# Performance work log

Hardware: AMD Instinct MI355X
Metric: run time of the kernel (lower is better)

Reference implementation:

```python
import jax, jax.numpy as jnp
import numpy as np

B, T, H = 32, 1024, 1024


def setup_inputs() -> dict:
    key = jax.random.key(0)
    k1, k2, k3, k4, k5 = jax.random.split(key, 5)
    h_t = jax.random.normal(k1, (B, H), dtype=jnp.float32)
    enc_out = jax.random.normal(k2, (B, T, H), dtype=jnp.float32)
    src_mask = jnp.ones((B, T), dtype=bool)
    s = 1.0 / np.sqrt(H)
    Wa = jax.random.normal(k3, (H, H), dtype=jnp.float32) * s
    Ua = jax.random.normal(k4, (H, H), dtype=jnp.float32) * s
    va = jax.random.normal(k5, (H,), dtype=jnp.float32) * s
    return {"h_t": h_t, "enc_out": enc_out, "src_mask": src_mask,
            "Wa": Wa, "Ua": Ua, "va": va}


def reference(h_t, enc_out, src_mask, Wa, Ua, va):
    # h_proj: [B,H] ; enc_proj: [B,T,H]
    h_proj = h_t @ Wa.T
    enc_proj = jnp.einsum('bth,kh->btk', enc_out, Ua)
    # additive score: va . tanh(Wa h + Ua enc)  -> [B,T]
    e = jnp.einsum('bth,h->bt', jnp.tanh(h_proj[:, None, :] + enc_proj), va)
    e = jnp.where(src_mask, e, -jnp.inf)
    attn = jax.nn.softmax(e, axis=1)                     # [B,T]
    context = jnp.einsum('bt,bth->bh', attn, enc_out)    # [B,H]
    return context, attn
```

## Files before the change

### kernel.cpp

```cpp
#include <hip/hip_runtime.h>

#define BB 32
#define TT 1024
#define HH 1024
#define MM (BB * TT)

typedef __bf16 bf16x8 __attribute__((ext_vector_type(8)));
typedef float  f32x4  __attribute__((ext_vector_type(4)));

__device__ __forceinline__ void async_copy16(const void* g, void* l) {
  __builtin_amdgcn_global_load_lds(
      (const __attribute__((address_space(1))) void*)g,
      (__attribute__((address_space(3))) void*)l, 16, 0, 0);
}

__device__ __forceinline__ float fast_tanh(float x) {
  float e2 = __expf(2.f * x);
  return 1.f - 2.f * __builtin_amdgcn_rcpf(e2 + 1.f);
}

__global__ __launch_bounds__(256) void mini_prep_kernel(
    const float* __restrict__ Ua, const float* __restrict__ h_t,
    const float* __restrict__ Wa, __bf16* __restrict__ uab,
    float* __restrict__ hp, float* __restrict__ e) {
  const int blk = blockIdx.x;
  const int tid = threadIdx.x;

  if (blk < 128) {
    const int b = blk >> 2;
    const int k = (blk & 3) * 256 + tid;
    __shared__ float hs[HH];
    for (int i = tid; i < HH; i += 256) hs[i] = h_t[b * HH + i];
    __syncthreads();
    const float4* w  = (const float4*)(Wa + (size_t)k * HH);
    const float4* hv = (const float4*)hs;
    float acc = 0.f;
#pragma unroll 8
    for (int i = 0; i < HH / 4; ++i) {
      float4 a = w[i];
      float4 h = hv[i];
      acc += a.x * h.x + a.y * h.y + a.z * h.z + a.w * h.w;
    }
    hp[b * HH + k] = acc;
  } else if (blk < 256) {
    int F = (blk - 128) * 256 + tid;
#pragma unroll
    for (int it = 0; it < 4; ++it, F += 32768) {
      const int c   = F & 2047;
      const int t   = F >> 11;
      const int kt  = t & 15;
      const int rt  = t >> 4;
      const int u   = c >> 10;
      const int idx = (c >> 3) & 127;
      const int s   = c & 7;
      const int g   = s ^ (idx & 7);
      const int row = (idx & 63) + ((idx >> 6) & 1) * 128 + u * 64;
      const float* sp = Ua + (((size_t)rt * 256 + row) << 10) + (kt << 6) + (g << 3);
      f32x4 a  = *(const f32x4*)sp;
      f32x4 b2 = *(const f32x4*)(sp + 4);
      bf16x8 o;
      o[0] = (__bf16)a[0];  o[1] = (__bf16)a[1];
      o[2] = (__bf16)a[2];  o[3] = (__bf16)a[3];
      o[4] = (__bf16)b2[0]; o[5] = (__bf16)b2[1];
      o[6] = (__bf16)b2[2]; o[7] = (__bf16)b2[3];
      *(bf16x8*)(uab + (size_t)F * 8) = o;
    }
  } else {
    f32x4 z = {0.f, 0.f, 0.f, 0.f};
    f32x4* ep = (f32x4*)e;
#pragma unroll
    for (int i = 0; i < 32; ++i) ep[i * 256 + tid] = z;
  }
}

__global__ __launch_bounds__(128) void hproj_kernel(
    const float* __restrict__ h_t, const float* __restrict__ Wa,
    float* __restrict__ hp) {
  const int k = blockIdx.x * 128 + threadIdx.x;
  const int b = blockIdx.y;
  __shared__ float hs[HH];
  for (int i = threadIdx.x; i < HH; i += 128) hs[i] = h_t[b * HH + i];
  __syncthreads();
  const float4* w  = (const float4*)(Wa + (size_t)k * HH);
  const float4* hv = (const float4*)hs;
  float acc = 0.f;
#pragma unroll 8
  for (int i = 0; i < HH / 4; ++i) {
    float4 a = w[i];
    float4 h = hv[i];
    acc += a.x * h.x + a.y * h.y + a.z * h.z + a.w * h.w;
  }
  hp[b * HH + k] = acc;
}

__global__ __launch_bounds__(512, 1) void score_8ph_kernel(
    const float* __restrict__ enc, const __bf16* __restrict__ uab,
    const float* __restrict__ hp, const float* __restrict__ va,
    float* __restrict__ e) {
  __shared__ __bf16 As[2][16384];
  __shared__ __bf16 Bs[2][16384];

  const int wg = blockIdx.x;
  const int sw = (wg & 7) * 64 + (wg >> 3);
  const int nt = sw & 3;
  const int mt = sw >> 2;
  const int b  = mt >> 2;

  const int tid  = threadIdx.x;
  const int lane = tid & 63;
  const int wid  = tid >> 6;
  const int wr   = wid >> 2;
  const int wc   = wid & 3;
  const int rl   = lane & 15;
  const int kq   = lane >> 4;
  const int e7   = rl & 7;

  const float* Af = enc + ((size_t)(mt * 256) << 10);
  const __bf16* Bg = uab + ((size_t)(nt * 16) << 14);

  const int aidx = tid >> 3;
  const int ag8  = ((tid & 7) ^ (aidx & 7)) << 3;

  const int s0 = ((kq ^ e7) << 4);
  const int s1 = (((kq + 4) ^ e7) << 4);
  const int arow = (rl + wr * 64) * 128;
  const int brow = (rl + (wc >> 1) * 64) * 128 + (wc & 1) * 16384;

#define LDA(buf, mi, sl) (*(const bf16x8*)((const char*)(buf) + \
    (((mi) >> 2) * 16384 + ((mi) & 3) * 2048) + arow + (sl)))
#define LDB(buf, nj, sl) (*(const bf16x8*)((const char*)(buf) + \
    ((nj) * 2048) + brow + (sl)))

#define BSTAGE(kt2, lp, u) do { \
    const __bf16* _g = Bg + (((size_t)(kt2)) << 14) + (((u) << 10) + tid) * 8; \
    __bf16* _l = (lp) + (((u) << 10) + tid) * 8; \
    async_copy16(_g, _l); \
    async_copy16(_g + 4096, _l + 4096); \
  } while (0)

#define ALOAD(ra, rb, rc, rd, kt2, u) do { \
    const float* _p1 = Af + ((size_t)(aidx + (u) * 64) << 10) + ((kt2) << 6) + ag8; \
    const float* _p2 = _p1 + (128 << 10); \
    ra = *(const f32x4*)_p1; rb = *(const f32x4*)(_p1 + 4); \
    rc = *(const f32x4*)_p2; rd = *(const f32x4*)(_p2 + 4); \
  } while (0)

#define AWRITE(lp, u, ra, rb, rc, rd) do { \
    __bf16* _l = (lp) + ((u) << 13) + tid * 8; \
    bf16x8 o1, o2; \
    o1[0] = (__bf16)ra[0]; o1[1] = (__bf16)ra[1]; \
    o1[2] = (__bf16)ra[2]; o1[3] = (__bf16)ra[3]; \
    o1[4] = (__bf16)rb[0]; o1[5] = (__bf16)rb[1]; \
    o1[6] = (__bf16)rb[2]; o1[7] = (__bf16)rb[3]; \
    o2[0] = (__bf16)rc[0]; o2[1] = (__bf16)rc[1]; \
    o2[2] = (__bf16)rc[2]; o2[3] = (__bf16)rc[3]; \
    o2[4] = (__bf16)rd[0]; o2[5] = (__bf16)rd[1]; \
    o2[6] = (__bf16)rd[2]; o2[7] = (__bf16)rd[3]; \
    *(bf16x8*)_l = o1; \
    *(bf16x8*)(_l + 4096) = o2; \
  } while (0)

#define MFMA16(ml, kkb) do { \
    _Pragma("unroll") \
    for (int nj = 0; nj < 4; ++nj) { \
      acc[(ml) + 0][nj] = __builtin_amdgcn_mfma_f32_16x16x32_bf16(af0, bfr[(kkb) + nj], acc[(ml) + 0][nj], 0, 0, 0); \
      acc[(ml) + 1][nj] = __builtin_amdgcn_mfma_f32_16x16x32_bf16(af1, bfr[(kkb) + nj], acc[(ml) + 1][nj], 0, 0, 0); \
      acc[(ml) + 2][nj] = __builtin_amdgcn_mfma_f32_16x16x32_bf16(af2, bfr[(kkb) + nj], acc[(ml) + 2][nj], 0, 0, 0); \
      acc[(ml) + 3][nj] = __builtin_amdgcn_mfma_f32_16x16x32_bf16(af3, bfr[(kkb) + nj], acc[(ml) + 3][nj], 0, 0, 0); \
    } \
  } while (0)

  f32x4 acc[8][4] = {};
  bf16x8 bfr[8];
  f32x4 xa, xb, xc, xd;
  f32x4 ya, yb, yc, yd;

  ALOAD(xa, xb, xc, xd, 0, 0);
  BSTAGE(0, &Bs[0][0], 0);
  BSTAGE(0, &Bs[0][0], 1);
  ALOAD(ya, yb, yc, yd, 0, 1);
  BSTAGE(1, &Bs[1][0], 0);
  BSTAGE(1, &Bs[1][0], 1);
  asm volatile("s_waitcnt vmcnt(4)" ::: "memory");
  AWRITE(&As[0][0], 0, xa, xb, xc, xd);
  AWRITE(&As[0][0], 1, ya, yb, yc, yd);
  ALOAD(xa, xb, xc, xd, 1, 0);
  asm volatile("s_waitcnt lgkmcnt(0)" ::: "memory");
  __builtin_amdgcn_s_barrier();

  for (int t = 0; t < 15; ++t) {
    const int p = t & 1;
    const char* Ab = (const char*)&As[p][0];
    const char* Bb = (const char*)&Bs[p][0];
    __bf16* An = &As[p ^ 1][0];

    {
#pragma unroll
      for (int nj = 0; nj < 4; ++nj) { bfr[nj] = LDB(Bb, nj, s0); bfr[4 + nj] = LDB(Bb, nj, s1); }
      bf16x8 af0 = LDA(Ab, 0, s0), af1 = LDA(Ab, 1, s0), af2 = LDA(Ab, 2, s0), af3 = LDA(Ab, 3, s0);
      ALOAD(ya, yb, yc, yd, t + 1, 1);
      __builtin_amdgcn_s_barrier();
      asm volatile("s_waitcnt lgkmcnt(0)" ::: "memory");
      __builtin_amdgcn_s_setprio(1);
      MFMA16(0, 0);
      __builtin_amdgcn_s_setprio(0);
      __builtin_amdgcn_s_barrier();
    }
    {
      bf16x8 af0 = LDA(Ab, 0, s1), af1 = LDA(Ab, 1, s1), af2 = LDA(Ab, 2, s1), af3 = LDA(Ab, 3, s1);
      if (t < 14) BSTAGE(t + 2, &Bs[p][0], 0);
      __builtin_amdgcn_s_barrier();
      asm volatile("s_waitcnt lgkmcnt(0)" ::: "memory");
      __builtin_amdgcn_s_setprio(1);
      MFMA16(0, 4);
      __builtin_amdgcn_s_setprio(0);
      __builtin_amdgcn_s_barrier();
    }
    {
      bf16x8 af0 = LDA(Ab, 4, s0), af1 = LDA(Ab, 5, s0), af2 = LDA(Ab, 6, s0), af3 = LDA(Ab, 7, s0);
      if (t < 14) BSTAGE(t + 2, &Bs[p][0], 1);
      __builtin_amdgcn_s_barrier();
      asm volatile("s_waitcnt lgkmcnt(0)" ::: "memory");
      __builtin_amdgcn_s_setprio(1);
      MFMA16(4, 0);
      __builtin_amdgcn_s_setprio(0);
      __builtin_amdgcn_s_barrier();
    }
    {
      bf16x8 af0 = LDA(Ab, 4, s1), af1 = LDA(Ab, 5, s1), af2 = LDA(Ab, 6, s1), af3 = LDA(Ab, 7, s1);
      __builtin_amdgcn_s_barrier();
      asm volatile("s_waitcnt lgkmcnt(0)" ::: "memory");
      __builtin_amdgcn_s_setprio(1);
      MFMA16(4, 4);
      __builtin_amdgcn_s_setprio(0);
      if (t < 14) asm volatile("s_waitcnt vmcnt(4)" ::: "memory");
      else        asm volatile("s_waitcnt vmcnt(0)" ::: "memory");
      AWRITE(An, 0, xa, xb, xc, xd);
      AWRITE(An, 1, ya, yb, yc, yd);
      if (t < 14) ALOAD(xa, xb, xc, xd, t + 2, 0);
      asm volatile("s_waitcnt lgkmcnt(0)" ::: "memory");
      __builtin_amdgcn_s_barrier();
    }
  }

  {
    const char* Ab = (const char*)&As[1][0];
    const char* Bb = (const char*)&Bs[1][0];
    {
#pragma unroll
      for (int nj = 0; nj < 4; ++nj) { bfr[nj] = LDB(Bb, nj, s0); bfr[4 + nj] = LDB(Bb, nj, s1); }
      bf16x8 af0 = LDA(Ab, 0, s0), af1 = LDA(Ab, 1, s0), af2 = LDA(Ab, 2, s0), af3 = LDA(Ab, 3, s0);
      __builtin_amdgcn_s_barrier();
      asm volatile("s_waitcnt lgkmcnt(0)" ::: "memory");
      __builtin_amdgcn_s_setprio(1);
      MFMA16(0, 0);
      __builtin_amdgcn_s_setprio(0);
      __builtin_amdgcn_s_barrier();
    }
    {
      bf16x8 af0 = LDA(Ab, 0, s1), af1 = LDA(Ab, 1, s1), af2 = LDA(Ab, 2, s1), af3 = LDA(Ab, 3, s1);
      __builtin_amdgcn_s_barrier();
      asm volatile("s_waitcnt lgkmcnt(0)" ::: "memory");
      __builtin_amdgcn_s_setprio(1);
      MFMA16(0, 4);
      __builtin_amdgcn_s_setprio(0);
      __builtin_amdgcn_s_barrier();
    }
    {
      bf16x8 af0 = LDA(Ab, 4, s0), af1 = LDA(Ab, 5, s0), af2 = LDA(Ab, 6, s0), af3 = LDA(Ab, 7, s0);
      __builtin_amdgcn_s_barrier();
      asm volatile("s_waitcnt lgkmcnt(0)" ::: "memory");
      __builtin_amdgcn_s_setprio(1);
      MFMA16(4, 0);
      __builtin_amdgcn_s_setprio(0);
      __builtin_amdgcn_s_barrier();
    }
    {
      bf16x8 af0 = LDA(Ab, 4, s1), af1 = LDA(Ab, 5, s1), af2 = LDA(Ab, 6, s1), af3 = LDA(Ab, 7, s1);
      __builtin_amdgcn_s_barrier();
      asm volatile("s_waitcnt lgkmcnt(0)" ::: "memory");
      __builtin_amdgcn_s_setprio(1);
      MFMA16(4, 4);
      __builtin_amdgcn_s_setprio(0);
    }
  }

  const float* hpb = hp + (b << 10);
#pragma unroll
  for (int mi = 0; mi < 8; ++mi) {
    float rs[4] = {0.f, 0.f, 0.f, 0.f};
#pragma unroll
    for (int nj = 0; nj < 4; ++nj) {
      const int col  = nt * 256 + wc * 64 + nj * 16 + rl;
      const float hv = hpb[col];
      const float vv = va[col];
#pragma unroll
      for (int j = 0; j < 4; ++j)
        rs[j] += fast_tanh(acc[mi][nj][j] + hv) * vv;
    }
#pragma unroll
    for (int j = 0; j < 4; ++j) {
      float r = rs[j];
      r += __shfl_xor(r, 1);
      r += __shfl_xor(r, 2);
      r += __shfl_xor(r, 4);
      r += __shfl_xor(r, 8);
      if (rl == 0)
        atomicAdd(&e[mt * 256 + wr * 128 + mi * 16 + kq * 4 + j], r);
    }
  }
#undef LDA
#undef LDB
#undef BSTAGE
#undef ALOAD
#undef AWRITE
#undef MFMA16
}

#define BM 128
#define BN 128
#define BK 32

__device__ __forceinline__ bf16x8 cvt8(const float* p) {
  f32x4 a = *(const f32x4*)p;
  f32x4 b = *(const f32x4*)(p + 4);
  bf16x8 r;
  r[0] = (__bf16)a[0]; r[1] = (__bf16)a[1]; r[2] = (__bf16)a[2]; r[3] = (__bf16)a[3];
  r[4] = (__bf16)b[0]; r[5] = (__bf16)b[1]; r[6] = (__bf16)b[2]; r[7] = (__bf16)b[3];
  return r;
}

__device__ __forceinline__ void score_epilogue(
    f32x4 acc[4][4], int m0, int n0, int b, int lane, int wr, int wc,
    const float* __restrict__ hp, const float* __restrict__ va,
    float* __restrict__ e) {
  const int rl = lane & 15;
  const int rq = lane >> 4;
#pragma unroll
  for (int mi = 0; mi < 4; ++mi) {
    float rs[4] = {0.f, 0.f, 0.f, 0.f};
#pragma unroll
    for (int nj = 0; nj < 4; ++nj) {
      const int col  = n0 + wc * 64 + nj * 16 + rl;
      const float hv = hp[(b << 10) + col];
      const float vv = va[col];
#pragma unroll
      for (int j = 0; j < 4; ++j)
        rs[j] += fast_tanh(acc[mi][nj][j] + hv) * vv;
    }
#pragma unroll
    for (int j = 0; j < 4; ++j) {
      float r = rs[j];
      r += __shfl_xor(r, 1);
      r += __shfl_xor(r, 2);
      r += __shfl_xor(r, 4);
      r += __shfl_xor(r, 8);
      if (rl == 0)
        atomicAdd(&e[m0 + wr * 64 + mi * 16 + rq * 4 + j], r);
    }
  }
}

__global__ __launch_bounds__(256) void score_f32_kernel(
    const float* __restrict__ enc, const float* __restrict__ Ua,
    const float* __restrict__ hp, const float* __restrict__ va,
    float* __restrict__ e) {
  const int m0 = blockIdx.x * BM;
  const int n0 = blockIdx.y * BN;
  const int b  = m0 >> 10;

  __shared__ float As[BM * BK];
  __shared__ float Bs[BN * BK];

  const int tid  = threadIdx.x;
  const int lane = tid & 63;
  const int wid  = tid >> 6;
  const int wr   = wid >> 1;
  const int wc   = wid & 1;

  f32x4 acc[4][4] = {};

  const int srow = tid >> 3;
  const int scol = (tid & 7) * 4;
  const float* gA = enc + (((size_t)(m0 + srow)) << 10) + scol;
  const float* gB = Ua  + (((size_t)(n0 + srow)) << 10) + scol;
  float* lA = As + srow * BK + scol;
  float* lB = Bs + srow * BK + scol;

  for (int kt = 0; kt < HH / BK; ++kt) {
    const int h0 = kt * BK;
    __syncthreads();
#pragma unroll
    for (int i = 0; i < 4; ++i) {
      async_copy16(gA + ((size_t)(i * 32) << 10) + h0, lA + i * 32 * BK);
      async_copy16(gB + ((size_t)(i * 32) << 10) + h0, lB + i * 32 * BK);
    }
    __syncthreads();

    const int koff = (lane >> 4) * 8;
    const int rl   = lane & 15;
    bf16x8 af[4], bfr[4];
#pragma unroll
    for (int mi = 0; mi < 4; ++mi)
      af[mi] = cvt8(As + (wr * 64 + mi * 16 + rl) * BK + koff);
#pragma unroll
    for (int nj = 0; nj < 4; ++nj)
      bfr[nj] = cvt8(Bs + (wc * 64 + nj * 16 + rl) * BK + koff);
#pragma unroll
    for (int mi = 0; mi < 4; ++mi)
#pragma unroll
      for (int nj = 0; nj < 4; ++nj)
        acc[mi][nj] = __builtin_amdgcn_mfma_f32_16x16x32_bf16(
            af[mi], bfr[nj], acc[mi][nj], 0, 0, 0);
  }

  score_epilogue(acc, m0, n0, b, lane, wr, wc, hp, va, e);
}

__global__ __launch_bounds__(256) void softmax_kernel(
    const float* __restrict__ e, const int* __restrict__ mask,
    float* __restrict__ attn) {
  const int b   = blockIdx.x;
  const int tid = threadIdx.x;
  const float* eb = e + (b << 10);
  const int*   mb = mask + (b << 10);
  float v[4];
  float mx = -INFINITY;
#pragma unroll
  for (int j = 0; j < 4; ++j) {
    const int t = tid + j * 256;
    float x = mb[t] ? eb[t] : -INFINITY;
    v[j] = x;
    mx = fmaxf(mx, x);
  }
#pragma unroll
  for (int s = 1; s < 64; s <<= 1) mx = fmaxf(mx, __shfl_xor(mx, s));
  __shared__ float redm[4];
  if ((tid & 63) == 0) redm[tid >> 6] = mx;
  __syncthreads();
  mx = fmaxf(fmaxf(redm[0], redm[1]), fmaxf(redm[2], redm[3]));

  float s = 0.f;
#pragma unroll
  for (int j = 0; j < 4; ++j) { v[j] = __expf(v[j] - mx); s += v[j]; }
#pragma unroll
  for (int st = 1; st < 64; st <<= 1) s += __shfl_xor(s, st);
  __shared__ float reds[4];
  if ((tid & 63) == 0) reds[tid >> 6] = s;
  __syncthreads();
  s = reds[0] + reds[1] + reds[2] + reds[3];
  const float inv = 1.f / s;
#pragma unroll
  for (int j = 0; j < 4; ++j) attn[(b << 10) + tid + j * 256] = v[j] * inv;
}

__global__ __launch_bounds__(256) void context_f32_kernel(
    const float* __restrict__ enc, const float* __restrict__ attn,
    float* __restrict__ ctx) {
  const int q   = blockIdx.x;
  const int b   = blockIdx.y;
  const int tid = threadIdx.x;
  const int h4  = tid & 31;
  const int tg  = tid >> 5;

  __shared__ float at[1024];
  for (int i = tid; i < 1024; i += 256) at[i] = attn[(b << 10) + i];
  __syncthreads();

  const float* ebase = enc + ((size_t)b << 20) + ((size_t)(tg * 128) << 10)
                       + q * 128 + h4 * 4;
  const float* ap = at + tg * 128;
  f32x4 acc = {0.f, 0.f, 0.f, 0.f};
#pragma unroll 4
  for (int t = 0; t < 128; ++t) {
    f32x4 v = *(const f32x4*)(ebase + ((size_t)t << 10));
    const float w = ap[t];
    acc[0] += w * v[0]; acc[1] += w * v[1];
    acc[2] += w * v[2]; acc[3] += w * v[3];
  }

  __shared__ f32x4 red[8][32];
  red[tg][h4] = acc;
  __syncthreads();

  if (tid < 32) {
    f32x4 s = red[0][tid];
#pragma unroll
    for (int r = 1; r < 8; ++r) {
      f32x4 v = red[r][tid];
      s[0] += v[0]; s[1] += v[1]; s[2] += v[2]; s[3] += v[3];
    }
    *(f32x4*)(ctx + (b << 10) + q * 128 + tid * 4) = s;
  }
}

__global__ __launch_bounds__(256) void context_kernel(
    const float* __restrict__ attn, const float* __restrict__ enc,
    float* __restrict__ ctx) {
  const int h  = blockIdx.x * 256 + threadIdx.x;
  const int b  = blockIdx.y;
  const int t0 = blockIdx.z * 128;
  const float* ab = attn + (b << 10) + t0;
  const float* eb = enc + (((size_t)(b << 10) + t0) << 10) + h;
  float acc = 0.f;
#pragma unroll 4
  for (int t = 0; t < 128; ++t)
    acc = fmaf(ab[t], eb[(size_t)t << 10], acc);
  atomicAdd(&ctx[(b << 10) + h], acc);
}

extern "C" void kernel_launch(void* const* d_in, const int* in_sizes, int n_in,
                              void* d_out, int out_size, void* d_ws, size_t ws_size,
                              hipStream_t stream) {
  const float* h_t  = (const float*)d_in[0];
  const float* enc  = (const float*)d_in[1];
  const int*   mask = (const int*)d_in[2];
  const float* Wa   = (const float*)d_in[3];
  const float* Ua   = (const float*)d_in[4];
  const float* va   = (const float*)d_in[5];

  float* out = (float*)d_out;
  float* e   = (float*)d_ws;
  float* hp  = e + MM;

  const size_t base  = 2 * (size_t)MM * sizeof(float);
  const size_t uab_n = (size_t)HH * HH;
  const size_t need  = base + uab_n * sizeof(__bf16);

  if (ws_size >= need) {
    __bf16* uab = (__bf16*)((char*)d_ws + base);
    mini_prep_kernel<<<257, 256, 0, stream>>>(Ua, h_t, Wa, uab, hp, e);
    score_8ph_kernel<<<512, 512, 0, stream>>>(enc, uab, hp, va, e);
    softmax_kernel<<<BB, 256, 0, stream>>>(e, mask, out + BB * HH);
    context_f32_kernel<<<dim3(8, BB), 256, 0, stream>>>(enc, out + BB * HH, out);
  } else {
    hipMemsetAsync(e, 0, MM * sizeof(float), stream);
    hipMemsetAsync(out, 0, BB * HH * sizeof(float), stream);
    hproj_kernel<<<dim3(HH / 128, BB), 128, 0, stream>>>(h_t, Wa, hp);
    score_f32_kernel<<<dim3(MM / BM, HH / BN), 256, 0, stream>>>(enc, Ua, hp, va, e);
    softmax_kernel<<<BB, 256, 0, stream>>>(e, mask, out + BB * HH);
    context_kernel<<<dim3(HH / 256, BB, 8), 256, 0, stream>>>(out + BB * HH, enc, out);
  }
}
```

Baseline: 137.7 us.

## Fuse softmax into context kernel and re-stage GEMM loads across phases

Removes the separate softmax launch. Each context block now recomputes the row softmax from the raw scores and mask, and block q==0 writes the attention output. The score GEMM main loop is also rescheduled: B-fragment LDS reads are split across the first two phases, and the next-tile global loads and A LDS writes are spread over phases three and four with adjusted vmcnt waits. This saves one kernel launch and aims for better overlap of memory and MFMA work, at the cost of redundant softmax work (8x per batch row) and a riskier hand-tuned waitcnt schedule.

New measurement: 160.6 us. +16.7%, slower.

```diff
diff --git a/kernel.cpp b/kernel.cpp
--- a/kernel.cpp
+++ b/kernel.cpp
@@ -175,13 +175,13 @@
   f32x4 xa, xb, xc, xd;
   f32x4 ya, yb, yc, yd;
 
-  ALOAD(xa, xb, xc, xd, 0, 0);
   BSTAGE(0, &Bs[0][0], 0);
   BSTAGE(0, &Bs[0][0], 1);
-  ALOAD(ya, yb, yc, yd, 0, 1);
   BSTAGE(1, &Bs[1][0], 0);
   BSTAGE(1, &Bs[1][0], 1);
-  asm volatile("s_waitcnt vmcnt(4)" ::: "memory");
+  ALOAD(xa, xb, xc, xd, 0, 0);
+  ALOAD(ya, yb, yc, yd, 0, 1);
+  asm volatile("s_waitcnt vmcnt(0)" ::: "memory");
   AWRITE(&As[0][0], 0, xa, xb, xc, xd);
   AWRITE(&As[0][0], 1, ya, yb, yc, yd);
   ALOAD(xa, xb, xc, xd, 1, 0);
@@ -196,7 +196,7 @@
 
     {
 #pragma unroll
-      for (int nj = 0; nj < 4; ++nj) { bfr[nj] = LDB(Bb, nj, s0); bfr[4 + nj] = LDB(Bb, nj, s1); }
+      for (int nj = 0; nj < 4; ++nj) bfr[nj] = LDB(Bb, nj, s0);
       bf16x8 af0 = LDA(Ab, 0, s0), af1 = LDA(Ab, 1, s0), af2 = LDA(Ab, 2, s0), af3 = LDA(Ab, 3, s0);
       ALOAD(ya, yb, yc, yd, t + 1, 1);
       __builtin_amdgcn_s_barrier();
@@ -207,8 +207,9 @@
       __builtin_amdgcn_s_barrier();
     }
     {
+#pragma unroll
+      for (int nj = 0; nj < 4; ++nj) bfr[4 + nj] = LDB(Bb, nj, s1);
       bf16x8 af0 = LDA(Ab, 0, s1), af1 = LDA(Ab, 1, s1), af2 = LDA(Ab, 2, s1), af3 = LDA(Ab, 3, s1);
-      if (t < 14) BSTAGE(t + 2, &Bs[p][0], 0);
       __builtin_amdgcn_s_barrier();
       asm volatile("s_waitcnt lgkmcnt(0)" ::: "memory");
       __builtin_amdgcn_s_setprio(1);
@@ -218,7 +219,13 @@
     }
     {
       bf16x8 af0 = LDA(Ab, 4, s0), af1 = LDA(Ab, 5, s0), af2 = LDA(Ab, 6, s0), af3 = LDA(Ab, 7, s0);
-      if (t < 14) BSTAGE(t + 2, &Bs[p][0], 1);
+      if (t < 14) {
+        BSTAGE(t + 2, &Bs[p][0], 0);
+        asm volatile("s_waitcnt vmcnt(6)" ::: "memory");
+      } else {
+        asm volatile("s_waitcnt vmcnt(4)" ::: "memory");
+      }
+      AWRITE(An, 0, xa, xb, xc, xd);
       __builtin_amdgcn_s_barrier();
       asm volatile("s_waitcnt lgkmcnt(0)" ::: "memory");
       __builtin_amdgcn_s_setprio(1);
@@ -228,17 +235,19 @@
     }
     {
       bf16x8 af0 = LDA(Ab, 4, s1), af1 = LDA(Ab, 5, s1), af2 = LDA(Ab, 6, s1), af3 = LDA(Ab, 7, s1);
+      if (t < 14) {
+        BSTAGE(t + 2, &Bs[p][0], 1);
+        ALOAD(xa, xb, xc, xd, t + 2, 0);
+        asm volatile("s_waitcnt vmcnt(8)" ::: "memory");
+      } else {
+        asm volatile("s_waitcnt vmcnt(0)" ::: "memory");
+      }
+      AWRITE(An, 1, ya, yb, yc, yd);
       __builtin_amdgcn_s_barrier();
       asm volatile("s_waitcnt lgkmcnt(0)" ::: "memory");
       __builtin_amdgcn_s_setprio(1);
       MFMA16(4, 4);
       __builtin_amdgcn_s_setprio(0);
-      if (t < 14) asm volatile("s_waitcnt vmcnt(4)" ::: "memory");
-      else        asm volatile("s_waitcnt vmcnt(0)" ::: "memory");
-      AWRITE(An, 0, xa, xb, xc, xd);
-      AWRITE(An, 1, ya, yb, yc, yd);
-      if (t < 14) ALOAD(xa, xb, xc, xd, t + 2, 0);
-      asm volatile("s_waitcnt lgkmcnt(0)" ::: "memory");
       __builtin_amdgcn_s_barrier();
     }
   }
@@ -248,7 +257,7 @@
     const char* Bb = (const char*)&Bs[1][0];
     {
 #pragma unroll
-      for (int nj = 0; nj < 4; ++nj) { bfr[nj] = LDB(Bb, nj, s0); bfr[4 + nj] = LDB(Bb, nj, s1); }
+      for (int nj = 0; nj < 4; ++nj) bfr[nj] = LDB(Bb, nj, s0);
       bf16x8 af0 = LDA(Ab, 0, s0), af1 = LDA(Ab, 1, s0), af2 = LDA(Ab, 2, s0), af3 = LDA(Ab, 3, s0);
       __builtin_amdgcn_s_barrier();
       asm volatile("s_waitcnt lgkmcnt(0)" ::: "memory");
@@ -258,6 +267,8 @@
       __builtin_amdgcn_s_barrier();
     }
     {
+#pragma unroll
+      for (int nj = 0; nj < 4; ++nj) bfr[4 + nj] = LDB(Bb, nj, s1);
       bf16x8 af0 = LDA(Ab, 0, s1), af1 = LDA(Ab, 1, s1), af2 = LDA(Ab, 2, s1), af3 = LDA(Ab, 3, s1);
       __builtin_amdgcn_s_barrier();
       asm volatile("s_waitcnt lgkmcnt(0)" ::: "memory");
@@ -454,29 +465,63 @@
   for (int j = 0; j < 4; ++j) attn[(b << 10) + tid + j * 256] = v[j] * inv;
 }
 
-__global__ __launch_bounds__(256) void context_f32_kernel(
-    const float* __restrict__ enc, const float* __restrict__ attn,
+__global__ __launch_bounds__(256) void context_sm_kernel(
+    const float* __restrict__ enc, const float* __restrict__ e,
+    const int* __restrict__ mask, float* __restrict__ attn,
     float* __restrict__ ctx) {
   const int q   = blockIdx.x;
   const int b   = blockIdx.y;
   const int tid = threadIdx.x;
-  const int h4  = tid & 31;
-  const int tg  = tid >> 5;
 
   __shared__ float at[1024];
-  for (int i = tid; i < 1024; i += 256) at[i] = attn[(b << 10) + i];
-  __syncthreads();
-
+  const float* eb = e + (b << 10);
+  const int*   mb = mask + (b << 10);
+  float v[4];
+  float mx = -INFINITY;
+#pragma unroll
+  for (int j = 0; j < 4; ++j) {
+    const int t = tid + j * 256;
+    float x = mb[t] ? eb[t] : -INFINITY;
+    v[j] = x;
+    mx = fmaxf(mx, x);
+  }
+#pragma unroll
+  for (int s = 1; s < 64; s <<= 1) mx = fmaxf(mx, __shfl_xor(mx, s));
+  __shared__ float redm[4];
+  if ((tid & 63) == 0) redm[tid >> 6] = mx;
+  __syncthreads();
+  mx = fmaxf(fmaxf(redm[0], redm[1]), fmaxf(redm[2], redm[3]));
+  float s = 0.f;
+#pragma unroll
+  for (int j = 0; j < 4; ++j) { v[j] = __expf(v[j] - mx); s += v[j]; }
+#pragma unroll
+  for (int st = 1; st < 64; st <<= 1) s += __shfl_xor(s, st);
+  __shared__ float reds[4];
+  if ((tid & 63) == 0) reds[tid >> 6] = s;
+  __syncthreads();
+  s = reds[0] + reds[1] + reds[2] + reds[3];
+  const float inv = 1.f / s;
+#pragma unroll
+  for (int j = 0; j < 4; ++j) {
+    const int t = tid + j * 256;
+    const float a = v[j] * inv;
+    at[t] = a;
+    if (q == 0) attn[(b << 10) + t] = a;
+  }
+  __syncthreads();
+
+  const int h4 = tid & 31;
+  const int tg = tid >> 5;
   const float* ebase = enc + ((size_t)b << 20) + ((size_t)(tg * 128) << 10)
                        + q * 128 + h4 * 4;
   const float* ap = at + tg * 128;
   f32x4 acc = {0.f, 0.f, 0.f, 0.f};
 #pragma unroll 4
   for (int t = 0; t < 128; ++t) {
-    f32x4 v = *(const f32x4*)(ebase + ((size_t)t << 10));
+    f32x4 w4 = *(const f32x4*)(ebase + ((size_t)t << 10));
     const float w = ap[t];
-    acc[0] += w * v[0]; acc[1] += w * v[1];
-    acc[2] += w * v[2]; acc[3] += w * v[3];
+    acc[0] += w * w4[0]; acc[1] += w * w4[1];
+    acc[2] += w * w4[2]; acc[3] += w * w4[3];
   }
 
   __shared__ f32x4 red[8][32];
@@ -484,13 +529,13 @@
   __syncthreads();
 
   if (tid < 32) {
-    f32x4 s = red[0][tid];
+    f32x4 sm = red[0][tid];
 #pragma unroll
     for (int r = 1; r < 8; ++r) {
-      f32x4 v = red[r][tid];
-      s[0] += v[0]; s[1] += v[1]; s[2] += v[2]; s[3] += v[3];
-    }
-    *(f32x4*)(ctx + (b << 10) + q * 128 + tid * 4) = s;
+      f32x4 w4 = red[r][tid];
+      sm[0] += w4[0]; sm[1] += w4[1]; sm[2] += w4[2]; sm[3] += w4[3];
+    }
+    *(f32x4*)(ctx + (b << 10) + q * 128 + tid * 4) = sm;
   }
 }
 
@@ -531,8 +576,8 @@
     __bf16* uab = (__bf16*)((char*)d_ws + base);
     mini_prep_kernel<<<257, 256, 0, stream>>>(Ua, h_t, Wa, uab, hp, e);
     score_8ph_kernel<<<512, 512, 0, stream>>>(enc, uab, hp, va, e);
-    softmax_kernel<<<BB, 256, 0, stream>>>(e, mask, out + BB * HH);
-    context_f32_kernel<<<dim3(8, BB), 256, 0, stream>>>(enc, out + BB * HH, out);
+    context_sm_kernel<<<dim3(8, BB), 256, 0, stream>>>(
+        enc, e, mask, out + BB * HH, out);
   } else {
     hipMemsetAsync(e, 0, MM * sizeof(float), stream);
     hipMemsetAsync(out, 0, BB * HH * sizeof(float), stream);
```
